# Optimization experiments

Measured on AMD Instinct MI355X. Metric: run time of the kernel, lower is better.

Reference implementation:

```python
import jax, jax.numpy as jnp
import numpy as np

B, NUM, LENTH, AUX = 32, 64, 64, 64
SIZE, OUT = 256, 256
IN_G = (LENTH + 1) * 2 + AUX  # 194


def _linear_params(k, fan_in, fan_out):
    # torch nn.Linear default init: U(-1/sqrt(fan_in), 1/sqrt(fan_in))
    s = 1.0 / np.sqrt(fan_in)
    kw, kb = jax.random.split(k)
    W = jax.random.uniform(kw, (fan_in, fan_out), minval=-s, maxval=s, dtype=jnp.float32)
    b = jax.random.uniform(kb, (fan_out,), minval=-s, maxval=s, dtype=jnp.float32)
    return W, b


def setup_inputs() -> dict:
    key = jax.random.key(0)
    ks = jax.random.split(key, 8)
    inp = {"x_aux": jax.random.normal(ks[0], (B, NUM, LENTH + AUX), dtype=jnp.float32)}
    dims = [("g1", IN_G, SIZE), ("g2", SIZE, SIZE), ("g3", SIZE, SIZE), ("g4", SIZE, OUT),
            ("f1", OUT, SIZE), ("f2", SIZE, SIZE), ("f3", SIZE, OUT)]
    for k, (name, fi, fo) in zip(ks[1:], dims):
        W, b = _linear_params(k, fi, fo)
        inp[name + "_w"] = W
        inp[name + "_b"] = b
    return inp


def reference(x_aux, g1_w, g1_b, g2_w, g2_b, g3_w, g3_b, g4_w, g4_b,
              f1_w, f1_b, f2_w, f2_b, f3_w, f3_b):
    bsz = x_aux.shape[0]
    # coord feature = object index i
    coord = jnp.broadcast_to(
        jnp.arange(NUM, dtype=x_aux.dtype)[None, :, None], (bsz, NUM, 1))
    x = jnp.concatenate([x_aux[:, :, :LENTH], coord], axis=-1)      # [B, N, LENTH+1]
    xa = jnp.concatenate([x_aux, coord], axis=-1)                   # [B, N, LENTH+AUX+1]
    # all-pairs broadcast+concat -> [B, N, N, IN_G]
    x_i = jnp.broadcast_to(x[:, None, :, :], (bsz, NUM, NUM, LENTH + 1))
    x_j = jnp.broadcast_to(xa[:, :, None, :], (bsz, NUM, NUM, LENTH + AUX + 1))
    pairs = jnp.concatenate([x_i, x_j], axis=-1)
    # shared g-MLP over every pair
    h = jax.nn.relu(pairs @ g1_w + g1_b)
    h = jax.nn.relu(h @ g2_w + g2_b)
    h = jax.nn.relu(h @ g3_w + g3_b)
    h = jax.nn.relu(h @ g4_w + g4_b)
    # sum-pool over all N*N pairs -> [B, OUT]
    x_g = h.sum(axis=(1, 2))
    # f-MLP (dropout treated as identity / eval mode)
    x_f = jax.nn.relu(x_g @ f1_w + f1_b)
    x_f = jax.nn.relu(x_f @ f2_w + f2_b)
    return x_f @ f3_w + f3_b
```

## Files before the change

kernel.cpp:

```cpp
#include <hip/hip_runtime.h>

#define BATCH 32
#define NOBJ  64
#define PADK  264

typedef _Float16 f16x4 __attribute__((ext_vector_type(4)));
typedef _Float16 f16x8 __attribute__((ext_vector_type(8)));
typedef float    f32x4 __attribute__((ext_vector_type(4)));
typedef float    f32x16 __attribute__((ext_vector_type(16)));

#define MFMA32(a, b, c) __builtin_amdgcn_mfma_f32_32x32x16_f16((a), (b), (c), 0, 0, 0)

__global__ __launch_bounds__(256) void prep_weights(
    const float* __restrict__ g1w, const float* __restrict__ g2w,
    const float* __restrict__ g3w, const float* __restrict__ g4w,
    _Float16* __restrict__ wtf, float* __restrict__ xg) {
  __shared__ _Float16 tile[256][33];
  const int blk = blockIdx.x;
  const int t = threadIdx.x;
  xg[blk * 256 + t] = 0.0f;

  const int l  = blk >> 3;
  const int nt = blk & 7;
  const float* src = (l == 0) ? g1w : (l == 1) ? g2w : (l == 2) ? g3w : g4w;

  const int nn = t & 31, kb = t >> 5;
#pragma unroll 4
  for (int pass = 0; pass < 32; ++pass) {
    int kn = pass * 8 + kb;
    int ok;
    if (l == 0) {
      if (kn < 64)        ok = kn;
      else if (kn < 192)  ok = kn + 1;
      else if (kn == 192) ok = 64;
      else if (kn == 193) ok = 193;
      else                ok = -1;
    } else {
      ok = kn;
    }
    float v = (ok >= 0) ? src[(size_t)ok * 256 + nt * 32 + nn] : 0.0f;
    tile[kn][nn] = (_Float16)v;
  }
  __syncthreads();

  const int lane = t & 63;
  const int nfrag = lane & 31;
  const int kbase = (lane >> 5) * 8;
  _Float16* dst = wtf + ((size_t)(l * 8 + nt) * 16) * 512;
#pragma unroll
  for (int q = 0; q < 4; ++q) {
    int kk = (t >> 6) + 4 * q;
    f16x8 fr;
#pragma unroll
    for (int j = 0; j < 8; ++j)
      fr[j] = tile[kk * 16 + kbase + j][nfrag];
    *(f16x8*)(dst + (size_t)kk * 512 + lane * 8) = fr;
  }
}

template <int STEPS>
__device__ __forceinline__ void do_layer(
    const _Float16* __restrict__ bp0, const _Float16* __restrict__ bp1,
    const _Float16* __restrict__ arow, f32x16 acc[8]) {
  f16x8 b0[STEPS], b1[STEPS];
#pragma unroll
  for (int kk = 0; kk < STEPS; ++kk) {
    b0[kk] = *(const f16x8*)(bp0 + kk * 512);
    b1[kk] = *(const f16x8*)(bp1 + kk * 512);
  }
#pragma unroll
  for (int kk = 0; kk < STEPS; ++kk) {
#pragma unroll
    for (int m = 0; m < 4; ++m) {
      f16x8 a = *(const f16x8*)(arow + (size_t)m * 32 * PADK + kk * 16);
      acc[m * 2]     = MFMA32(a, b0[kk], acc[m * 2]);
      acc[m * 2 + 1] = MFMA32(a, b1[kk], acc[m * 2 + 1]);
    }
  }
}

__global__ __launch_bounds__(256, 2) void g_mlp_pool(
    const float* __restrict__ x_aux,
    const _Float16* __restrict__ wtf,
    const float* __restrict__ g1b, const float* __restrict__ g2b,
    const float* __restrict__ g3b, const float* __restrict__ g4b,
    float* __restrict__ xg) {
  __shared__ _Float16 As[128][PADK];

  const int b  = blockIdx.x >> 5;
  const int i0 = (blockIdx.x & 31) * 2;
  const int t  = threadIdx.x;

  {
    const float* xb = x_aux + (size_t)b * NOBJ * 128;
    {
      const int c4 = t & 15, r0 = t >> 4;
#pragma unroll
      for (int it = 0; it < 8; ++it) {
        int r = it * 16 + r0;
        f32x4 v = *(const f32x4*)(xb + (size_t)(r & 63) * 128 + c4 * 4);
        f16x4 hh = {(_Float16)v[0], (_Float16)v[1], (_Float16)v[2], (_Float16)v[3]};
        *(f16x4*)&As[r][c4 * 4] = hh;
      }
    }
    {
      const int row = t >> 1, seg = t & 1;
      const int ir = i0 + (row >> 6);
      const float* xi = xb + (size_t)ir * 128;
#pragma unroll
      for (int u = 0; u < 8; ++u) {
        int c = seg * 64 + u * 8;
        f32x4 v0 = *(const f32x4*)(xi + c);
        f32x4 v1 = *(const f32x4*)(xi + c + 4);
        f16x8 hh = {(_Float16)v0[0], (_Float16)v0[1], (_Float16)v0[2], (_Float16)v0[3],
                    (_Float16)v1[0], (_Float16)v1[1], (_Float16)v1[2], (_Float16)v1[3]};
        *(f16x8*)&As[row][64 + c] = hh;
      }
      f16x8 z = {};
      *(f16x8*)&As[row][192 + seg * 32]     = z;
      *(f16x8*)&As[row][192 + seg * 32 + 8] = z;
      if (seg == 0) {
        As[row][192] = (_Float16)(row & 63);
        As[row][193] = (_Float16)ir;
      }
    }
  }
  __syncthreads();

  const int lane = t & 63;
  const int wave = t >> 6;
  const int c31  = lane & 31;
  const int h    = lane >> 5;
  const int n0   = wave * 64;
  const float* gb[4] = {g1b, g2b, g3b, g4b};

  for (int layer = 0; layer < 4; ++layer) {
    const float bv0 = gb[layer][n0 + c31];
    const float bv1 = gb[layer][n0 + 32 + c31];

    f32x16 acc[8] = {};

    const _Float16* bp0 =
        wtf + ((size_t)(layer * 8 + wave * 2) * 16) * 512 + lane * 8;
    const _Float16* bp1 = bp0 + 16 * 512;
    const _Float16* arow = &As[c31][h * 8];

    if (layer == 0)
      do_layer<13>(bp0, bp1, arow, acc);
    else
      do_layer<16>(bp0, bp1, arow, acc);

    if (layer < 3) {
      __syncthreads();
#pragma unroll
      for (int m = 0; m < 4; ++m)
#pragma unroll
        for (int g = 0; g < 4; ++g)
#pragma unroll
          for (int r = 0; r < 4; ++r) {
            const int row = m * 32 + g * 8 + h * 4 + r;
            const int reg = g * 4 + r;
            As[row][n0 + c31]      = (_Float16)fmaxf(acc[m * 2][reg] + bv0, 0.f);
            As[row][n0 + 32 + c31] = (_Float16)fmaxf(acc[m * 2 + 1][reg] + bv1, 0.f);
          }
      __syncthreads();
    } else {
      float s0 = 0.f, s1 = 0.f;
#pragma unroll
      for (int m = 0; m < 4; ++m)
#pragma unroll
        for (int reg = 0; reg < 16; ++reg) {
          s0 += fmaxf(acc[m * 2][reg] + bv0, 0.f);
          s1 += fmaxf(acc[m * 2 + 1][reg] + bv1, 0.f);
        }
      s0 += __shfl_xor(s0, 32, 64);
      s1 += __shfl_xor(s1, 32, 64);
      if (h == 0) {
        atomicAdd(&xg[b * 256 + n0 + c31], s0);
        atomicAdd(&xg[b * 256 + n0 + 32 + c31], s1);
      }
    }
  }
}

__global__ __launch_bounds__(1024) void f_mlp(
    const float* __restrict__ xg,
    const float* __restrict__ f1w, const float* __restrict__ f1b,
    const float* __restrict__ f2w, const float* __restrict__ f2b,
    const float* __restrict__ f3w, const float* __restrict__ f3b,
    float* __restrict__ out) {
  __shared__ float xs[256], ys[256], ps[4][256];
  const int b = blockIdx.x;
  const int t = threadIdx.x;
  const int n = t & 255;
  const int kc = t >> 8;

  if (t < 256) xs[t] = xg[b * 256 + t];
  __syncthreads();

  float p = 0.f;
#pragma unroll 8
  for (int k0 = 0; k0 < 64; ++k0) {
    int k = kc * 64 + k0;
    p += xs[k] * f1w[k * 256 + n];
  }
  ps[kc][n] = p;
  __syncthreads();
  if (t < 256)
    ys[t] = fmaxf(f1b[t] + ps[0][t] + ps[1][t] + ps[2][t] + ps[3][t], 0.f);
  __syncthreads();

  p = 0.f;
#pragma unroll 8
  for (int k0 = 0; k0 < 64; ++k0) {
    int k = kc * 64 + k0;
    p += ys[k] * f2w[k * 256 + n];
  }
  ps[kc][n] = p;
  __syncthreads();
  if (t < 256)
    xs[t] = fmaxf(f2b[t] + ps[0][t] + ps[1][t] + ps[2][t] + ps[3][t], 0.f);
  __syncthreads();

  p = 0.f;
#pragma unroll 8
  for (int k0 = 0; k0 < 64; ++k0) {
    int k = kc * 64 + k0;
    p += xs[k] * f3w[k * 256 + n];
  }
  ps[kc][n] = p;
  __syncthreads();
  if (t < 256)
    out[b * 256 + t] = f3b[t] + ps[0][t] + ps[1][t] + ps[2][t] + ps[3][t];
}

extern "C" void kernel_launch(void* const* d_in, const int* in_sizes, int n_in,
                              void* d_out, int out_size, void* d_ws, size_t ws_size,
                              hipStream_t stream) {
  const float* x_aux = (const float*)d_in[0];
  const float* g1w = (const float*)d_in[1];
  const float* g1b = (const float*)d_in[2];
  const float* g2w = (const float*)d_in[3];
  const float* g2b = (const float*)d_in[4];
  const float* g3w = (const float*)d_in[5];
  const float* g3b = (const float*)d_in[6];
  const float* g4w = (const float*)d_in[7];
  const float* g4b = (const float*)d_in[8];
  const float* f1w = (const float*)d_in[9];
  const float* f1b = (const float*)d_in[10];
  const float* f2w = (const float*)d_in[11];
  const float* f2b = (const float*)d_in[12];
  const float* f3w = (const float*)d_in[13];
  const float* f3b = (const float*)d_in[14];
  float* out = (float*)d_out;

  _Float16* wtf = (_Float16*)d_ws;
  float* xg = (float*)((char*)d_ws + 4u * 256u * 256u * 2u);

  hipLaunchKernelGGL(prep_weights, dim3(32), dim3(256), 0, stream,
                     g1w, g2w, g3w, g4w, wtf, xg);
  hipLaunchKernelGGL(g_mlp_pool, dim3(BATCH * 32), dim3(256), 0, stream,
                     x_aux, wtf, g1b, g2b, g3b, g4b, xg);
  hipLaunchKernelGGL(f_mlp, dim3(BATCH), dim3(1024), 0, stream,
                     xg, f1w, f1b, f2w, f2b, f3w, f3b, out);
}
```

Before: 164.1 us.

## Retile g-MLP waves to 64x128 blocks with permuted hidden columns and B prefetch

Each wave now computes a 64-row by 128-column output tile instead of 128 rows by 64 columns. A operands are read from LDS half as often per MFMA, while B fragments are loaded four at a time. The weight prep permutes the K order of layers 2-4 so each lane can write four adjacent fp16 activations as one packed f16x4 LDS store instead of scattered scalar stores. B loads switch from preloading every K step to a one-step-ahead double buffer, which cuts register pressure but exposes more global-load latency.

```diff
diff --git a/kernel.cpp b/kernel.cpp
--- a/kernel.cpp
+++ b/kernel.cpp
@@ -10,6 +10,7 @@
 typedef float    f32x16 __attribute__((ext_vector_type(16)));
 
 #define MFMA32(a, b, c) __builtin_amdgcn_mfma_f32_32x32x16_f16((a), (b), (c), 0, 0, 0)
+
 
 __global__ __launch_bounds__(256) void prep_weights(
     const float* __restrict__ g1w, const float* __restrict__ g2w,
@@ -20,33 +21,34 @@
   const int t = threadIdx.x;
   xg[blk * 256 + t] = 0.0f;
 
-  const int l  = blk >> 3;
-  const int nt = blk & 7;
+  const int l = blk >> 3;
+  const int s = blk & 7;
+  const int nbase = 128 * (s >> 2) + 32 * (s & 3);
   const float* src = (l == 0) ? g1w : (l == 1) ? g2w : (l == 2) ? g3w : g4w;
 
   const int nn = t & 31, kb = t >> 5;
 #pragma unroll 4
   for (int pass = 0; pass < 32; ++pass) {
-    int kn = pass * 8 + kb;
-    int ok;
+    int kp = pass * 8 + kb;
+    int kl;
     if (l == 0) {
-      if (kn < 64)        ok = kn;
-      else if (kn < 192)  ok = kn + 1;
-      else if (kn == 192) ok = 64;
-      else if (kn == 193) ok = 193;
-      else                ok = -1;
+      if (kp < 64)        kl = kp;
+      else if (kp < 192)  kl = kp + 1;
+      else if (kp == 192) kl = 64;
+      else if (kp == 193) kl = 193;
+      else                kl = -1;
     } else {
-      ok = kn;
-    }
-    float v = (ok >= 0) ? src[(size_t)ok * 256 + nt * 32 + nn] : 0.0f;
-    tile[kn][nn] = (_Float16)v;
+      kl = 128 * (kp >> 7) + ((kp & 127) >> 2) + 32 * (kp & 3);
+    }
+    float v = (kl >= 0) ? src[(size_t)kl * 256 + nbase + nn] : 0.0f;
+    tile[kp][nn] = (_Float16)v;
   }
   __syncthreads();
 
   const int lane = t & 63;
   const int nfrag = lane & 31;
   const int kbase = (lane >> 5) * 8;
-  _Float16* dst = wtf + ((size_t)(l * 8 + nt) * 16) * 512;
+  _Float16* dst = wtf + ((size_t)(l * 8 + s) * 16) * 512;
 #pragma unroll
   for (int q = 0; q < 4; ++q) {
     int kk = (t >> 6) + 4 * q;
@@ -60,22 +62,29 @@
 
 template <int STEPS>
 __device__ __forceinline__ void do_layer(
-    const _Float16* __restrict__ bp0, const _Float16* __restrict__ bp1,
-    const _Float16* __restrict__ arow, f32x16 acc[8]) {
-  f16x8 b0[STEPS], b1[STEPS];
+    const _Float16* __restrict__ bp,
+    const _Float16* __restrict__ arow,
+    f32x16 acc[2][4]) {
+  f16x8 bc[4], bn[4];
+#pragma unroll
+  for (int ns = 0; ns < 4; ++ns)
+    bc[ns] = *(const f16x8*)(bp + (size_t)ns * 16 * 512);
 #pragma unroll
   for (int kk = 0; kk < STEPS; ++kk) {
-    b0[kk] = *(const f16x8*)(bp0 + kk * 512);
-    b1[kk] = *(const f16x8*)(bp1 + kk * 512);
-  }
-#pragma unroll
-  for (int kk = 0; kk < STEPS; ++kk) {
-#pragma unroll
-    for (int m = 0; m < 4; ++m) {
-      f16x8 a = *(const f16x8*)(arow + (size_t)m * 32 * PADK + kk * 16);
-      acc[m * 2]     = MFMA32(a, b0[kk], acc[m * 2]);
-      acc[m * 2 + 1] = MFMA32(a, b1[kk], acc[m * 2 + 1]);
-    }
+    if (kk < STEPS - 1) {
+#pragma unroll
+      for (int ns = 0; ns < 4; ++ns)
+        bn[ns] = *(const f16x8*)(bp + (size_t)ns * 16 * 512 + (kk + 1) * 512);
+    }
+    f16x8 a0 = *(const f16x8*)(arow + kk * 16);
+    f16x8 a1 = *(const f16x8*)(arow + (size_t)32 * PADK + kk * 16);
+#pragma unroll
+    for (int ns = 0; ns < 4; ++ns) {
+      acc[0][ns] = MFMA32(a0, bc[ns], acc[0][ns]);
+      acc[1][ns] = MFMA32(a1, bc[ns], acc[1][ns]);
+    }
+#pragma unroll
+    for (int ns = 0; ns < 4; ++ns) bc[ns] = bn[ns];
   }
 }
 
@@ -129,55 +138,63 @@
 
   const int lane = t & 63;
   const int wave = t >> 6;
+  const int mh   = wave & 1;
+  const int nh   = wave >> 1;
   const int c31  = lane & 31;
   const int h    = lane >> 5;
-  const int n0   = wave * 64;
+  const int R    = mh * 64;
   const float* gb[4] = {g1b, g2b, g3b, g4b};
 
   for (int layer = 0; layer < 4; ++layer) {
-    const float bv0 = gb[layer][n0 + c31];
-    const float bv1 = gb[layer][n0 + 32 + c31];
-
-    f32x16 acc[8] = {};
-
-    const _Float16* bp0 =
-        wtf + ((size_t)(layer * 8 + wave * 2) * 16) * 512 + lane * 8;
-    const _Float16* bp1 = bp0 + 16 * 512;
-    const _Float16* arow = &As[c31][h * 8];
+    float bv[4];
+#pragma unroll
+    for (int ns = 0; ns < 4; ++ns)
+      bv[ns] = gb[layer][nh * 128 + ns * 32 + c31];
+
+    f32x16 acc[2][4] = {};
+
+    const _Float16* bp =
+        wtf + ((size_t)(layer * 8 + nh * 4) * 16) * 512 + lane * 8;
+    const _Float16* arow = &As[R + c31][h * 8];
 
     if (layer == 0)
-      do_layer<13>(bp0, bp1, arow, acc);
+      do_layer<13>(bp, arow, acc);
     else
-      do_layer<16>(bp0, bp1, arow, acc);
+      do_layer<16>(bp, arow, acc);
 
     if (layer < 3) {
       __syncthreads();
 #pragma unroll
-      for (int m = 0; m < 4; ++m)
+      for (int m = 0; m < 2; ++m)
 #pragma unroll
         for (int g = 0; g < 4; ++g)
 #pragma unroll
           for (int r = 0; r < 4; ++r) {
-            const int row = m * 32 + g * 8 + h * 4 + r;
+            const int row = R + m * 32 + g * 8 + h * 4 + r;
             const int reg = g * 4 + r;
-            As[row][n0 + c31]      = (_Float16)fmaxf(acc[m * 2][reg] + bv0, 0.f);
-            As[row][n0 + 32 + c31] = (_Float16)fmaxf(acc[m * 2 + 1][reg] + bv1, 0.f);
+            f16x4 pk = {
+                (_Float16)fmaxf(acc[m][0][reg] + bv[0], 0.f),
+                (_Float16)fmaxf(acc[m][1][reg] + bv[1], 0.f),
+                (_Float16)fmaxf(acc[m][2][reg] + bv[2], 0.f),
+                (_Float16)fmaxf(acc[m][3][reg] + bv[3], 0.f)};
+            *(f16x4*)&As[row][nh * 128 + 4 * c31] = pk;
           }
       __syncthreads();
     } else {
-      float s0 = 0.f, s1 = 0.f;
-#pragma unroll
-      for (int m = 0; m < 4; ++m)
-#pragma unroll
-        for (int reg = 0; reg < 16; ++reg) {
-          s0 += fmaxf(acc[m * 2][reg] + bv0, 0.f);
-          s1 += fmaxf(acc[m * 2 + 1][reg] + bv1, 0.f);
-        }
-      s0 += __shfl_xor(s0, 32, 64);
-      s1 += __shfl_xor(s1, 32, 64);
+      float s[4] = {};
+#pragma unroll
+      for (int ns = 0; ns < 4; ++ns) {
+#pragma unroll
+        for (int m = 0; m < 2; ++m)
+#pragma unroll
+          for (int reg = 0; reg < 16; ++reg)
+            s[ns] += fmaxf(acc[m][ns][reg] + bv[ns], 0.f);
+        s[ns] += __shfl_xor(s[ns], 32, 64);
+      }
       if (h == 0) {
-        atomicAdd(&xg[b * 256 + n0 + c31], s0);
-        atomicAdd(&xg[b * 256 + n0 + 32 + c31], s1);
+#pragma unroll
+        for (int ns = 0; ns < 4; ++ns)
+          atomicAdd(&xg[b * 256 + nh * 128 + ns * 32 + c31], s[ns]);
       }
     }
   }
```

Result: slower. 177.3 us (+8.1%).
